# Kernel tuning notes

Measured on AMD Instinct MI355X. Metric: run time of the kernel, lower is better.

Reference implementation:

```python
import jax, jax.numpy as jnp
import numpy as np

D, H, C, T, B = 1024, 128, 256, 16, 8192


def setup_inputs() -> dict:
    key = jax.random.key(0)
    ks = jax.random.split(key, 7)
    s = 0.02
    return {
        "x": jax.random.normal(ks[0], (B, D), dtype=jnp.float32),
        "Wr": jax.random.normal(ks[1], (D, T), dtype=jnp.float32) * s,  # router weight (transposed vs torch)
        "br": jnp.zeros((T,), dtype=jnp.float32),
        "W1": jax.random.normal(ks[2], (T, D, H), dtype=jnp.float32) * s,  # per-task fc1
        "b1": jnp.zeros((T, H), dtype=jnp.float32),
        "W2": jax.random.normal(ks[3], (T, H, C), dtype=jnp.float32) * s,  # per-task fc2
        "b2": jnp.zeros((T, C), dtype=jnp.float32),
    }


def reference(x, Wr, br, W1, b1, W2, b2):
    # Router: softmax over tasks, [B, T]
    task_probs = jax.nn.softmax(x @ Wr + br, axis=1)
    # All task experts as one batched grouped-GEMM pass.
    h = jax.nn.relu(jnp.einsum("bd,tdh->tbh", x, W1) + b1[:, None, :])  # [T, B, H]
    preds = jnp.einsum("tbh,thc->tbc", h, W2) + b2[:, None, :]           # [T, B, C]
    # Weight each task's predictions by its routing probability.
    task_preds = preds * task_probs.T[:, :, None]                         # [T, B, C]
    return task_probs, task_preds
```

## Files before the change

kernel.cpp:

```cpp
#include <hip/hip_runtime.h>

using bf16x8 = __attribute__((ext_vector_type(8))) short;
using f32x4  = __attribute__((ext_vector_type(4))) float;

#define B_SZ 8192
#define D_SZ 1024
#define H_SZ 128
#define C_SZ 256
#define T_SZ 16

#define SB __builtin_amdgcn_sched_barrier(0)

__device__ __forceinline__ unsigned short f2bf(float f) {
  unsigned int u = __float_as_uint(f);
  return (unsigned short)((u + 0x7fffu + ((u >> 16) & 1u)) >> 16);
}

__global__ __launch_bounds__(256) void transpose_cast_kernel(const float* __restrict__ src,
                                                             unsigned short* __restrict__ dst,
                                                             int R, int C, int cshift) {
  __shared__ float tile[32][257];
  const int t = blockIdx.y;
  const int r0 = blockIdx.x * 32;
  const float* s = src + ((size_t)t * R + r0) * C;
  const int n = 32 * C;
  for (int idx = threadIdx.x; idx < n; idx += 256)
    tile[idx >> cshift][idx & (C - 1)] = s[idx];
  __syncthreads();
  unsigned short* d = dst + (size_t)t * C * R + r0;
  for (int idx = threadIdx.x; idx < n; idx += 256) {
    int cc = idx >> 5, rr = idx & 31;
    d[(size_t)cc * R + rr] = f2bf(tile[rr][cc]);
  }
}

__global__ __launch_bounds__(256) void router_cast_kernel(const float* __restrict__ x,
                                                          const float* __restrict__ Wr,
                                                          const float* __restrict__ br,
                                                          float* __restrict__ out0,
                                                          unsigned short* __restrict__ xb) {
  const int lane = threadIdx.x & 63;
  const int wid  = threadIdx.x >> 6;
  const int brow = blockIdx.x * 16 + wid * 4;
  float acc[4][16];
#pragma unroll
  for (int r = 0; r < 4; ++r)
#pragma unroll
    for (int tt = 0; tt < 16; ++tt) acc[r][tt] = 0.f;

  for (int it = 0; it < 16; ++it) {
    const int d = it * 64 + lane;
    const float4* w4 = (const float4*)(Wr + (size_t)d * 16);
    float4 wa = w4[0], wb = w4[1], wc = w4[2], wd = w4[3];
    const float wv[16] = {wa.x, wa.y, wa.z, wa.w, wb.x, wb.y, wb.z, wb.w,
                          wc.x, wc.y, wc.z, wc.w, wd.x, wd.y, wd.z, wd.w};
#pragma unroll
    for (int r = 0; r < 4; ++r) {
      const float xv = x[(size_t)(brow + r) * 1024 + d];
      xb[(size_t)(brow + r) * 1024 + d] = f2bf(xv);
#pragma unroll
      for (int tt = 0; tt < 16; ++tt) acc[r][tt] += xv * wv[tt];
    }
  }
#pragma unroll
  for (int off = 32; off >= 1; off >>= 1) {
#pragma unroll
    for (int r = 0; r < 4; ++r)
#pragma unroll
      for (int tt = 0; tt < 16; ++tt) acc[r][tt] += __shfl_xor(acc[r][tt], off);
  }
  if (lane == 0) {
#pragma unroll
    for (int r = 0; r < 4; ++r) {
      float v[16]; float m = -1e30f;
#pragma unroll
      for (int tt = 0; tt < 16; ++tt) { v[tt] = acc[r][tt] + br[tt]; m = fmaxf(m, v[tt]); }
      float ssum = 0.f;
#pragma unroll
      for (int tt = 0; tt < 16; ++tt) { v[tt] = __expf(v[tt] - m); ssum += v[tt]; }
      const float inv = 1.0f / ssum;
      float4* o = (float4*)(out0 + (size_t)(brow + r) * 16);
      o[0] = make_float4(v[0] * inv, v[1] * inv, v[2] * inv, v[3] * inv);
      o[1] = make_float4(v[4] * inv, v[5] * inv, v[6] * inv, v[7] * inv);
      o[2] = make_float4(v[8] * inv, v[9] * inv, v[10] * inv, v[11] * inv);
      o[3] = make_float4(v[12] * inv, v[13] * inv, v[14] * inv, v[15] * inv);
    }
  }
}

#define SW_REG 65536

__global__ __launch_bounds__(512, 2) void expert_kernel(
    const unsigned short* __restrict__ xb, const unsigned short* __restrict__ w1b,
    const unsigned short* __restrict__ w2b, const float* __restrict__ b1,
    const float* __restrict__ b2, const float* __restrict__ probs,
    float* __restrict__ out1) {
  __shared__ __align__(16) char smem[98304];
  const int tid  = threadIdx.x;
  const int lane = tid & 63;
  const int w    = tid >> 6;
  const int l16  = lane & 15;
  const int l4   = lane >> 4;

  const int bid = blockIdx.x;
  const int lid = (bid & 7) * 64 + (bid >> 3);
  const int t   = lid & 15;
  const int b0  = (lid >> 4) * 256;

  const unsigned short* gp[6];
  unsigned int ldo[6];
#pragma unroll
  for (int it = 0; it < 6; ++it) {
    if (it < 4) {
      const unsigned int o = (unsigned int)w * 4096u + (unsigned int)it * 1024u + (unsigned int)lane * 16u;
      const int row = (int)(o >> 7);
      const int cb  = (int)((o & 127u) ^ (((unsigned)row & 7u) << 4));
      gp[it]  = xb + (size_t)(b0 + row) * 1024 + (cb >> 1);
      ldo[it] = o;
    } else {
      const unsigned int o = (unsigned int)w * 2048u + (unsigned int)(it - 4) * 1024u + (unsigned int)lane * 16u;
      const int row = (int)(o >> 7);
      const int cb  = (int)((o & 127u) ^ (((unsigned)row & 7u) << 4));
      gp[it]  = w1b + (size_t)(t * 128 + row) * 1024 + (cb >> 1);
      ldo[it] = o;
    }
  }

#define STAGE(curbuf, kt)                                                              \
  {                                                                                    \
    _Pragma("unroll")                                                                  \
    for (int it = 0; it < 6; ++it) {                                                   \
      const unsigned short* g = gp[it] + (kt) * 64;                                    \
      char* dd = smem + (it < 4 ? (curbuf) * 32768 + (int)ldo[it]                      \
                                : SW_REG + (curbuf) * 16384 + (int)ldo[it]);           \
      __builtin_amdgcn_global_load_lds(                                                \
          (const __attribute__((address_space(1))) unsigned int*)g,                    \
          (__attribute__((address_space(3))) unsigned int*)dd, 16, 0, 0);              \
    }                                                                                  \
  }

  const int wn = w & 1;
  const int wm = w >> 1;
  f32x4 acc1[4][4] = {};

#define FC1_PHASE(curbuf, ks)                                                          \
  {                                                                                    \
    const int bx_base = (curbuf) * 32768;                                              \
    const int aw_base = SW_REG + (curbuf) * 16384;                                     \
    const int cb = (ks) * 64 + l4 * 16;                                                \
    bf16x8 aw[4], bx[4];                                                               \
    _Pragma("unroll")                                                                  \
    for (int ni = 0; ni < 4; ++ni) {                                                   \
      const int row = wn * 64 + ni * 16 + l16;                                         \
      aw[ni] = *(const bf16x8*)(smem + aw_base + (row << 7) + (cb ^ ((row & 7) << 4)));\
    }                                                                                  \
    _Pragma("unroll")                                                                  \
    for (int mi = 0; mi < 4; ++mi) {                                                   \
      const int row = wm * 64 + mi * 16 + l16;                                         \
      bx[mi] = *(const bf16x8*)(smem + bx_base + (row << 7) + (cb ^ ((row & 7) << 4)));\
    }                                                                                  \
    __builtin_amdgcn_s_setprio(1);                                                     \
    _Pragma("unroll")                                                                  \
    for (int ni = 0; ni < 4; ++ni)                                                     \
      _Pragma("unroll")                                                                \
      for (int mi = 0; mi < 4; ++mi)                                                   \
        acc1[ni][mi] = __builtin_amdgcn_mfma_f32_16x16x32_bf16(aw[ni], bx[mi], acc1[ni][mi], 0, 0, 0); \
    __builtin_amdgcn_s_setprio(0);                                                     \
  }

  STAGE(0, 0);
  STAGE(1, 1);
  asm volatile("s_waitcnt vmcnt(6)" ::: "memory");
  SB; __builtin_amdgcn_s_barrier(); SB;

#pragma unroll
  for (int kt = 0; kt < 14; ++kt) {
    const int cur = kt & 1;
    FC1_PHASE(cur, 0);
    FC1_PHASE(cur, 1);
    SB; __builtin_amdgcn_s_barrier(); SB;
    STAGE(cur, kt + 2);
    asm volatile("s_waitcnt vmcnt(6)" ::: "memory");
    SB; __builtin_amdgcn_s_barrier(); SB;
  }
  FC1_PHASE(0, 0);
  FC1_PHASE(0, 1);
  SB; __builtin_amdgcn_s_barrier(); SB;
  asm volatile("s_waitcnt vmcnt(0)" ::: "memory");
  SB; __builtin_amdgcn_s_barrier(); SB;
  FC1_PHASE(1, 0);
  FC1_PHASE(1, 1);
  SB; __builtin_amdgcn_s_barrier(); SB;

#pragma unroll
  for (int ni = 0; ni < 4; ++ni) {
    const int n0 = wn * 64 + ni * 16 + l4 * 4;
    float bb[4];
#pragma unroll
    for (int r = 0; r < 4; ++r) bb[r] = b1[t * 128 + n0 + r];
#pragma unroll
    for (int mi = 0; mi < 4; ++mi) {
      const int m = wm * 64 + mi * 16 + l16;
      unsigned int pk[2];
#pragma unroll
      for (int h = 0; h < 2; ++h) {
        float v0 = fmaxf(acc1[ni][mi][2 * h + 0] + bb[2 * h + 0], 0.f);
        float v1 = fmaxf(acc1[ni][mi][2 * h + 1] + bb[2 * h + 1], 0.f);
        pk[h] = (unsigned int)f2bf(v0) | ((unsigned int)f2bf(v1) << 16);
      }
      const int byte = (m << 8) + ((n0 * 2) ^ ((m & 7) << 4));
      *(uint2*)(smem + byte) = make_uint2(pk[0], pk[1]);
    }
  }
  asm volatile("s_waitcnt lgkmcnt(0)" ::: "memory");
  SB; __builtin_amdgcn_s_barrier(); SB;

  const int wm2 = w >> 1;
  const int wc  = w & 1;
  f32x4 acc2[4][8] = {};
  const unsigned short* w2t = w2b + (size_t)t * C_SZ * H_SZ;

#pragma unroll
  for (int ks = 0; ks < 4; ++ks) {
    const int cb = ks * 64 + l4 * 16;
    bf16x8 ah[4];
#pragma unroll
    for (int mi = 0; mi < 4; ++mi) {
      const int row = wm2 * 64 + mi * 16 + l16;
      ah[mi] = *(const bf16x8*)(smem + (row << 8) + (cb ^ ((row & 7) << 4)));
    }
#pragma unroll
    for (int ci = 0; ci < 8; ++ci) {
      const int c = wc * 128 + ci * 16 + l16;
      bf16x8 bw = *(const bf16x8*)(w2t + (size_t)c * 128 + ks * 32 + l4 * 8);
#pragma unroll
      for (int mi = 0; mi < 4; ++mi)
        acc2[mi][ci] = __builtin_amdgcn_mfma_f32_16x16x32_bf16(ah[mi], bw, acc2[mi][ci], 0, 0, 0);
    }
  }

  const size_t outbase = (size_t)t * (size_t)(B_SZ * C_SZ);
#pragma unroll
  for (int mi = 0; mi < 4; ++mi) {
    const int m0 = wm2 * 64 + mi * 16 + l4 * 4;
    float pv[4];
#pragma unroll
    for (int r = 0; r < 4; ++r) pv[r] = probs[(size_t)(b0 + m0 + r) * 16 + t];
#pragma unroll
    for (int ci = 0; ci < 8; ++ci) {
      const int c = wc * 128 + ci * 16 + l16;
      const float bias = b2[t * 256 + c];
#pragma unroll
      for (int r = 0; r < 4; ++r)
        out1[outbase + (size_t)(b0 + m0 + r) * 256 + c] = (acc2[mi][ci][r] + bias) * pv[r];
    }
  }
}

extern "C" void kernel_launch(void* const* d_in, const int* in_sizes, int n_in,
                              void* d_out, int out_size, void* d_ws, size_t ws_size,
                              hipStream_t stream) {
  const float* x  = (const float*)d_in[0];
  const float* Wr = (const float*)d_in[1];
  const float* br = (const float*)d_in[2];
  const float* W1 = (const float*)d_in[3];
  const float* b1 = (const float*)d_in[4];
  const float* W2 = (const float*)d_in[5];
  const float* b2 = (const float*)d_in[6];
  float* out0 = (float*)d_out;
  float* out1 = out0 + (size_t)B_SZ * T_SZ;

  char* ws = (char*)d_ws;
  unsigned short* xb  = (unsigned short*)ws;
  unsigned short* w1b = (unsigned short*)(ws + (size_t)16777216);
  unsigned short* w2b = (unsigned short*)(ws + (size_t)16777216 + 4194304);

  router_cast_kernel<<<B_SZ / 16, 256, 0, stream>>>(x, Wr, br, out0, xb);
  transpose_cast_kernel<<<dim3(D_SZ / 32, T_SZ), 256, 0, stream>>>(W1, w1b, D_SZ, H_SZ, 7);
  transpose_cast_kernel<<<dim3(H_SZ / 32, T_SZ), 256, 0, stream>>>(W2, w2b, H_SZ, C_SZ, 8);
  expert_kernel<<<512, 512, 0, stream>>>(xb, w1b, w2b, b1, b2, out0, out1);
}
```

Before: 104.2 us.

## Triple-buffer FC1 staging and interleave async loads with MFMA sub-phases

Moves the expert kernel's FC1 pipeline from double to triple buffering of the x and W1 tiles, so the next tile's loads have more lead time. Each k-tile is split into four sub-phases that interleave LDS reads, per-thread async global-to-LDS copies and groups of eight MFMAs, separated by barriers. Shared memory rises from 96KB to 144KB, and the hidden-activation buffer moves to a separate offset. The trade-off is that the larger LDS footprint likely allows only one 512-thread block per CU instead of two, and each tile now has many more barriers.

```diff
diff --git a/kernel.cpp b/kernel.cpp
--- a/kernel.cpp
+++ b/kernel.cpp
@@ -88,14 +88,15 @@
   }
 }
 
-#define SW_REG 65536
+#define SWB 98304
+#define SH_O 32768
 
 __global__ __launch_bounds__(512, 2) void expert_kernel(
     const unsigned short* __restrict__ xb, const unsigned short* __restrict__ w1b,
     const unsigned short* __restrict__ w2b, const float* __restrict__ b1,
     const float* __restrict__ b2, const float* __restrict__ probs,
     float* __restrict__ out1) {
-  __shared__ __align__(16) char smem[98304];
+  __shared__ __align__(16) char smem[147456];
   const int tid  = threadIdx.x;
   const int lane = tid & 63;
   const int w    = tid >> 6;
@@ -111,86 +112,91 @@
   unsigned int ldo[6];
 #pragma unroll
   for (int it = 0; it < 6; ++it) {
-    if (it < 4) {
-      const unsigned int o = (unsigned int)w * 4096u + (unsigned int)it * 1024u + (unsigned int)lane * 16u;
-      const int row = (int)(o >> 7);
-      const int cb  = (int)((o & 127u) ^ (((unsigned)row & 7u) << 4));
-      gp[it]  = xb + (size_t)(b0 + row) * 1024 + (cb >> 1);
-      ldo[it] = o;
-    } else {
-      const unsigned int o = (unsigned int)w * 2048u + (unsigned int)(it - 4) * 1024u + (unsigned int)lane * 16u;
-      const int row = (int)(o >> 7);
-      const int cb  = (int)((o & 127u) ^ (((unsigned)row & 7u) << 4));
-      gp[it]  = w1b + (size_t)(t * 128 + row) * 1024 + (cb >> 1);
-      ldo[it] = o;
-    }
-  }
-
-#define STAGE(curbuf, kt)                                                              \
-  {                                                                                    \
-    _Pragma("unroll")                                                                  \
-    for (int it = 0; it < 6; ++it) {                                                   \
-      const unsigned short* g = gp[it] + (kt) * 64;                                    \
-      char* dd = smem + (it < 4 ? (curbuf) * 32768 + (int)ldo[it]                      \
-                                : SW_REG + (curbuf) * 16384 + (int)ldo[it]);           \
-      __builtin_amdgcn_global_load_lds(                                                \
-          (const __attribute__((address_space(1))) unsigned int*)g,                    \
-          (__attribute__((address_space(3))) unsigned int*)dd, 16, 0, 0);              \
-    }                                                                                  \
+    const unsigned int o = (unsigned int)(it < 4 ? it : it - 4) * 8192u + (unsigned int)tid * 16u;
+    const int row = (int)(o >> 7);
+    const int cb  = (int)((o & 127u) ^ (((unsigned)row & 7u) << 4));
+    gp[it]  = (it < 4) ? (xb + (size_t)(b0 + row) * 1024 + (cb >> 1))
+                       : (w1b + (size_t)(t * 128 + row) * 1024 + (cb >> 1));
+    ldo[it] = o;
+  }
+
+#define STAGE1(it_, nbuf_, kt_)                                                        \
+  {                                                                                    \
+    const unsigned short* g = gp[it_] + (kt_) * 64;                                    \
+    char* dd = smem + ((it_) < 4 ? (nbuf_) * 32768 + (int)ldo[it_]                     \
+                                 : SWB + (nbuf_) * 16384 + (int)ldo[it_]);             \
+    __builtin_amdgcn_global_load_lds(                                                  \
+        (const __attribute__((address_space(1))) unsigned int*)g,                      \
+        (__attribute__((address_space(3))) unsigned int*)dd, 16, 0, 0);                \
   }
 
   const int wn = w & 1;
   const int wm = w >> 1;
   f32x4 acc1[4][4] = {};
-
-#define FC1_PHASE(curbuf, ks)                                                          \
-  {                                                                                    \
-    const int bx_base = (curbuf) * 32768;                                              \
-    const int aw_base = SW_REG + (curbuf) * 16384;                                     \
-    const int cb = (ks) * 64 + l4 * 16;                                                \
-    bf16x8 aw[4], bx[4];                                                               \
+  bf16x8 aw[2][4], bx[2][4];
+
+#define RD_AW(buf_, ks_)                                                               \
+  {                                                                                    \
+    const int cb = (ks_) * 64 + l4 * 16;                                               \
     _Pragma("unroll")                                                                  \
     for (int ni = 0; ni < 4; ++ni) {                                                   \
       const int row = wn * 64 + ni * 16 + l16;                                         \
-      aw[ni] = *(const bf16x8*)(smem + aw_base + (row << 7) + (cb ^ ((row & 7) << 4)));\
+      aw[ks_][ni] = *(const bf16x8*)(smem + SWB + (buf_) * 16384 + (row << 7) + (cb ^ ((row & 7) << 4))); \
     }                                                                                  \
-    _Pragma("unroll")                                                                  \
-    for (int mi = 0; mi < 4; ++mi) {                                                   \
-      const int row = wm * 64 + mi * 16 + l16;                                         \
-      bx[mi] = *(const bf16x8*)(smem + bx_base + (row << 7) + (cb ^ ((row & 7) << 4)));\
-    }                                                                                  \
+  }
+#define RD_BX(buf_, ks_, mi_)                                                          \
+  {                                                                                    \
+    const int cb = (ks_) * 64 + l4 * 16;                                               \
+    const int row = wm * 64 + (mi_) * 16 + l16;                                        \
+    bx[ks_][mi_] = *(const bf16x8*)(smem + (buf_) * 32768 + (row << 7) + (cb ^ ((row & 7) << 4))); \
+  }
+#define MFMA8(ks_, j_)                                                                 \
+  {                                                                                    \
     __builtin_amdgcn_s_setprio(1);                                                     \
     _Pragma("unroll")                                                                  \
-    for (int ni = 0; ni < 4; ++ni)                                                     \
-      _Pragma("unroll")                                                                \
-      for (int mi = 0; mi < 4; ++mi)                                                   \
-        acc1[ni][mi] = __builtin_amdgcn_mfma_f32_16x16x32_bf16(aw[ni], bx[mi], acc1[ni][mi], 0, 0, 0); \
+    for (int ni = 0; ni < 4; ++ni) {                                                   \
+      acc1[ni][2*(j_)]   = __builtin_amdgcn_mfma_f32_16x16x32_bf16(aw[ks_][ni], bx[ks_][2*(j_)],   acc1[ni][2*(j_)],   0, 0, 0); \
+      acc1[ni][2*(j_)+1] = __builtin_amdgcn_mfma_f32_16x16x32_bf16(aw[ks_][ni], bx[ks_][2*(j_)+1], acc1[ni][2*(j_)+1], 0, 0, 0); \
+    }                                                                                  \
     __builtin_amdgcn_s_setprio(0);                                                     \
   }
-
-  STAGE(0, 0);
-  STAGE(1, 1);
+#define BAR SB; __builtin_amdgcn_s_barrier(); SB
+
+#pragma unroll
+  for (int it = 0; it < 6; ++it) STAGE1(it, 0, 0);
+#pragma unroll
+  for (int it = 0; it < 6; ++it) STAGE1(it, 1, 1);
   asm volatile("s_waitcnt vmcnt(6)" ::: "memory");
-  SB; __builtin_amdgcn_s_barrier(); SB;
-
-#pragma unroll
-  for (int kt = 0; kt < 14; ++kt) {
-    const int cur = kt & 1;
-    FC1_PHASE(cur, 0);
-    FC1_PHASE(cur, 1);
-    SB; __builtin_amdgcn_s_barrier(); SB;
-    STAGE(cur, kt + 2);
-    asm volatile("s_waitcnt vmcnt(6)" ::: "memory");
-    SB; __builtin_amdgcn_s_barrier(); SB;
-  }
-  FC1_PHASE(0, 0);
-  FC1_PHASE(0, 1);
-  SB; __builtin_amdgcn_s_barrier(); SB;
-  asm volatile("s_waitcnt vmcnt(0)" ::: "memory");
-  SB; __builtin_amdgcn_s_barrier(); SB;
-  FC1_PHASE(1, 0);
-  FC1_PHASE(1, 1);
-  SB; __builtin_amdgcn_s_barrier(); SB;
+  BAR;
+
+  int buf = 0, nbuf = 2;
+  for (int kt = 0; kt < 16; ++kt) {
+    const bool st = (kt < 14);
+    RD_AW(buf, 0); RD_BX(buf, 0, 0); RD_BX(buf, 0, 1);
+    if (st) { STAGE1(0, nbuf, kt + 2); STAGE1(1, nbuf, kt + 2); }
+    BAR;
+    MFMA8(0, 0);
+    BAR;
+    RD_BX(buf, 0, 2); RD_BX(buf, 0, 3);
+    if (st) STAGE1(2, nbuf, kt + 2);
+    BAR;
+    MFMA8(0, 1);
+    BAR;
+    RD_AW(buf, 1); RD_BX(buf, 1, 0); RD_BX(buf, 1, 1);
+    if (st) { STAGE1(3, nbuf, kt + 2); STAGE1(4, nbuf, kt + 2); }
+    BAR;
+    MFMA8(1, 0);
+    BAR;
+    RD_BX(buf, 1, 2); RD_BX(buf, 1, 3);
+    if (st) STAGE1(5, nbuf, kt + 2);
+    BAR;
+    MFMA8(1, 1);
+    if (kt <= 13)      { asm volatile("s_waitcnt vmcnt(6)" ::: "memory"); }
+    else if (kt == 14) { asm volatile("s_waitcnt vmcnt(0)" ::: "memory"); }
+    BAR;
+    buf  = (buf == 2)  ? 0 : buf + 1;
+    nbuf = (nbuf == 2) ? 0 : nbuf + 1;
+  }
 
 #pragma unroll
   for (int ni = 0; ni < 4; ++ni) {
@@ -209,11 +215,11 @@
         pk[h] = (unsigned int)f2bf(v0) | ((unsigned int)f2bf(v1) << 16);
       }
       const int byte = (m << 8) + ((n0 * 2) ^ ((m & 7) << 4));
-      *(uint2*)(smem + byte) = make_uint2(pk[0], pk[1]);
+      *(uint2*)(smem + SH_O + byte) = make_uint2(pk[0], pk[1]);
     }
   }
   asm volatile("s_waitcnt lgkmcnt(0)" ::: "memory");
-  SB; __builtin_amdgcn_s_barrier(); SB;
+  BAR;
 
   const int wm2 = w >> 1;
   const int wc  = w & 1;
@@ -227,7 +233,7 @@
 #pragma unroll
     for (int mi = 0; mi < 4; ++mi) {
       const int row = wm2 * 64 + mi * 16 + l16;
-      ah[mi] = *(const bf16x8*)(smem + (row << 8) + (cb ^ ((row & 7) << 4)));
+      ah[mi] = *(const bf16x8*)(smem + SH_O + (row << 8) + (cb ^ ((row & 7) << 4)));
     }
 #pragma unroll
     for (int ci = 0; ci < 8; ++ci) {
```

New measurement: 108.2 us. 1.04x slower.
